# Performance work log

Measured on AMD Instinct MI355X. Metric: run time of the kernel, lower is better.

The kernel has to match this reference:

```python
import jax, jax.numpy as jnp
import numpy as np
import math

NUM_BUCKETS = 32
MAX_DISTANCE = 128
N_HEADS = 16
D_KV = 64


def _relative_position_bucket(relative_position, num_buckets=NUM_BUCKETS, max_distance=MAX_DISTANCE):
    # bidirectional (encoder) variant
    num_buckets //= 2
    relative_buckets = (relative_position > 0).astype(jnp.int32) * num_buckets
    rp = jnp.abs(relative_position)
    max_exact = num_buckets // 2
    is_small = rp < max_exact
    rp_large = max_exact + (
        jnp.log(jnp.maximum(rp, 1).astype(jnp.float32) / max_exact)
        / math.log(max_distance / max_exact)
        * (num_buckets - max_exact)
    ).astype(jnp.int32)
    rp_large = jnp.minimum(rp_large, num_buckets - 1)
    return relative_buckets + jnp.where(is_small, rp, rp_large)


def compute_bias(rel_bias, q_len, k_len):
    ctx = jnp.arange(q_len)[:, None]
    mem = jnp.arange(k_len)[None, :]
    buckets = _relative_position_bucket(mem - ctx)          # [q, k]
    values = rel_bias[buckets]                               # [q, k, h]
    return jnp.transpose(values, (2, 0, 1))[None]            # [1, h, q, k]


def setup_inputs() -> dict:
    key = jax.random.key(0)
    ks = jax.random.split(key, 6)
    d_model, inner = 1024, N_HEADS * D_KV
    s = 0.02
    return {
        "hidden_states": jax.random.normal(ks[0], (2, 2048, d_model), jnp.float32),
        "Wq": jax.random.normal(ks[1], (d_model, inner), jnp.float32) * s,
        "Wk": jax.random.normal(ks[2], (d_model, inner), jnp.float32) * s,
        "Wv": jax.random.normal(ks[3], (d_model, inner), jnp.float32) * s,
        "Wo": jax.random.normal(ks[4], (inner, d_model), jnp.float32) * s,
        "rel_bias": jax.random.normal(ks[5], (NUM_BUCKETS, N_HEADS), jnp.float32) * s,
    }


def reference(hidden_states, Wq, Wk, Wv, Wo, rel_bias):
    B, S, D = hidden_states.shape

    def split_heads(x):  # [B,S,inner] -> [B,H,S,dk]
        return x.reshape(B, S, N_HEADS, D_KV).transpose(0, 2, 1, 3)

    q = split_heads(hidden_states @ Wq)
    k = split_heads(hidden_states @ Wk)
    v = split_heads(hidden_states @ Wv)

    # T5 does NOT scale by 1/sqrt(d_kv)
    scores = jnp.einsum("bhqd,bhkd->bhqk", q, k)
    scores = scores + compute_bias(rel_bias, S, S)
    attn = jax.nn.softmax(scores, axis=-1)
    ctx = jnp.einsum("bhqk,bhkd->bhqd", attn, v)
    ctx = ctx.transpose(0, 2, 1, 3).reshape(B, S, N_HEADS * D_KV)
    return ctx @ Wo
```

## Files before the change

kernel.cpp:

```cpp
#include <hip/hip_runtime.h>
#include <hip/hip_bf16.h>

typedef __bf16 bf16x8 __attribute__((ext_vector_type(8)));
typedef __bf16 bf16x4 __attribute__((ext_vector_type(4)));
typedef float floatx4 __attribute__((ext_vector_type(4)));
using bf16 = __hip_bfloat16;

#define S_    2048
#define NHEAD 16
#define LOG2E 1.4426950408889634f

__device__ __forceinline__ void load_lds16(const bf16* g, void* lds) {
  __builtin_amdgcn_global_load_lds((const __attribute__((address_space(1))) void*)g,
                                   (__attribute__((address_space(3))) void*)lds, 16, 0, 0);
}

__global__ void prep_kernel(const float* __restrict__ hidden,
                            const float* __restrict__ wq, const float* __restrict__ wk,
                            const float* __restrict__ wv, const float* __restrict__ wo,
                            const float* __restrict__ rel_bias,
                            bf16* __restrict__ hbf, bf16* __restrict__ wt_qkv,
                            bf16* __restrict__ wt_o, float* __restrict__ btab) {
  __shared__ bf16 tile[32][33];
  int bx = blockIdx.x, t = threadIdx.x;
  if (bx < 2048) {
    int i = (bx * 256 + t) * 8;
    float4 v0 = *(const float4*)(hidden + i);
    float4 v1 = *(const float4*)(hidden + i + 4);
    bf16 o8[8] = {__float2bfloat16(v0.x), __float2bfloat16(v0.y),
                  __float2bfloat16(v0.z), __float2bfloat16(v0.w),
                  __float2bfloat16(v1.x), __float2bfloat16(v1.y),
                  __float2bfloat16(v1.z), __float2bfloat16(v1.w)};
    *(uint4*)(hbf + i) = *(const uint4*)o8;
  } else if (bx < 6144) {
    int mat = (bx - 2048) >> 10, tb = (bx - 2048) & 1023;
    int n0 = (tb & 31) * 32, k0 = (tb >> 5) * 32;
    const float* src = (mat == 0) ? wq : (mat == 1) ? wk : (mat == 2) ? wv : wo;
    bf16* dst = (mat == 3) ? wt_o : wt_qkv + mat * 1024 * 1024;
    int tx = t & 31, ty = t >> 5;
#pragma unroll
    for (int j = 0; j < 32; j += 8)
      tile[ty + j][tx] = __float2bfloat16(src[(k0 + ty + j) * 1024 + n0 + tx]);
    __syncthreads();
#pragma unroll
    for (int j = 0; j < 32; j += 8)
      dst[(n0 + ty + j) * 1024 + k0 + tx] = tile[tx][ty + j];
  } else {
    int idx = (bx - 6144) * 256 + t;
    int h = idx >> 12, j = idx & 4095;
    int delta = j - 2048;
    int rb = (delta > 0) ? 16 : 0;
    int rpa = delta < 0 ? -delta : delta;
    int bsmall;
    if (rpa < 8) {
      bsmall = rpa;
    } else {
      int lg = 25 - __clz(rpa * rpa);
      bsmall = 8 + lg;
      if (bsmall > 15) bsmall = 15;
    }
    btab[idx] = rel_bias[(rb + bsmall) * 16 + h] * LOG2E;
  }
}

__global__ __launch_bounds__(256) void gemm_qkv_kernel(const bf16* __restrict__ A,
                                                       const bf16* __restrict__ Bt,
                                                       bf16* __restrict__ qh,
                                                       bf16* __restrict__ kf,
                                                       bf16* __restrict__ vf) {
  const int K = 1024;
  __shared__ bf16 As[128 * 32];
  __shared__ bf16 Bs[128 * 32];
  int t = threadIdx.x;
  int m0 = blockIdx.y * 128, n0 = blockIdx.x * 128;
  int w = t >> 6, lane = t & 63, ln = lane & 15, quad = lane >> 4;
  int wr = w >> 1, wc = w & 1;
  floatx4 acc[4][4];
  floatx4 zero = {0.f, 0.f, 0.f, 0.f};
#pragma unroll
  for (int i = 0; i < 4; i++)
#pragma unroll
    for (int j = 0; j < 4; j++) acc[i][j] = zero;

  int r = t >> 2, c = (t & 3) * 8;
  const bf16* Ag = A + (long)(m0 + r) * K + c;
  const bf16* Bg = Bt + (long)(n0 + r) * K + c;
  char* ldsA0 = (char*)As + w * 1024;
  char* ldsA1 = ldsA0 + 4096;
  char* ldsB0 = (char*)Bs + w * 1024;
  char* ldsB1 = ldsB0 + 4096;

  for (int k0 = 0; k0 < K; k0 += 32) {
    load_lds16(Ag + k0, ldsA0);
    load_lds16(Ag + (long)64 * K + k0, ldsA1);
    load_lds16(Bg + k0, ldsB0);
    load_lds16(Bg + (long)64 * K + k0, ldsB1);
    __syncthreads();
    bf16x8 af[4], bfv[4];
#pragma unroll
    for (int i = 0; i < 4; i++)
      af[i] = *(const bf16x8*)&As[(wr * 64 + i * 16 + ln) * 32 + quad * 8];
#pragma unroll
    for (int j = 0; j < 4; j++)
      bfv[j] = *(const bf16x8*)&Bs[(wc * 64 + j * 16 + ln) * 32 + quad * 8];
#pragma unroll
    for (int i = 0; i < 4; i++)
#pragma unroll
      for (int j = 0; j < 4; j++)
        acc[i][j] = __builtin_amdgcn_mfma_f32_16x16x32_bf16(af[i], bfv[j], acc[i][j], 0, 0, 0);
    __syncthreads();
  }

  int nb = n0 + wc * 64;
  int type = nb >> 10, h = (nb >> 6) & 15;
  int b = (m0 >> 11);
  int sl0 = (m0 & 2047) + wr * 64;
  long bhbase = (long)((b * 16 + h)) * 131072;

  if (type == 0) {
#pragma unroll
    for (int i = 0; i < 4; i++)
#pragma unroll
      for (int j = 0; j < 4; j++) {
        int d = j * 16 + ln;
#pragma unroll
        for (int rr = 0; rr < 4; rr++) {
          int s = sl0 + i * 16 + quad * 4 + rr;
          qh[bhbase + (long)s * 64 + d] = __float2bfloat16(acc[i][j][rr]);
        }
      }
  } else if (type == 1) {
#pragma unroll
    for (int i = 0; i < 4; i++)
#pragma unroll
      for (int j = 0; j < 4; j++) {
        int d = j * 16 + ln;
        int dpart = (d >> 5) * 512 + ((d >> 3) & 3) * 128 + (d & 7);
        int kb = (sl0 + i * 16) * 64;
#pragma unroll
        for (int rr = 0; rr < 4; rr++)
          kf[bhbase + kb + dpart + (quad * 4 + rr) * 8] = __float2bfloat16(acc[i][j][rr]);
      }
  } else {
#pragma unroll
    for (int i = 0; i < 4; i++)
#pragma unroll
      for (int j = 0; j < 4; j++) {
        int off = (sl0 + (i >> 1) * 32) * 64 + j * 512 +
                  ((quad >> 1) + ((i & 1) << 1)) * 128 + ln * 8 + (quad & 1) * 4;
        bf16x4 pk = {(__bf16)acc[i][j][0], (__bf16)acc[i][j][1],
                     (__bf16)acc[i][j][2], (__bf16)acc[i][j][3]};
        *(bf16x4*)(vf + bhbase + off) = pk;
      }
  }
}

__global__ __launch_bounds__(256, 2) void attn_kernel(const bf16* __restrict__ qh,
                                                      const bf16* __restrict__ kf,
                                                      const bf16* __restrict__ vf,
                                                      const float* __restrict__ btab,
                                                      float* __restrict__ opart,
                                                      float* __restrict__ lpart) {
  __shared__ char KV[2][16384];
  __shared__ char PsRaw[4 * 2048];
  int t = threadIdx.x, w = t >> 6, lane = t & 63, ln = lane & 15, quad = lane >> 4;
  int bh = blockIdx.x, h = bh & 15;
  int qw = blockIdx.y * 128 + w * 32;
  int ks = blockIdx.z, kbase0 = ks * 1024;

  const bf16* qbase = qh + (long)bh * S_ * 64;
  const bf16* kfb = kf + (long)bh * S_ * 64 + (long)kbase0 * 64;
  const bf16* vfb = vf + (long)bh * S_ * 64 + (long)kbase0 * 64;
  const float* bt = btab + h * 4096;
  char* myPs = PsRaw + w * 2048;
  int lbo = quad * 256 + ln * 16;

  bf16x8 Qf[2][2];
#pragma unroll
  for (int g = 0; g < 2; g++) {
    const bf16* qr = qbase + (long)(qw + g * 16 + ln) * 64;
    Qf[g][0] = *(const bf16x8*)(qr + quad * 8);
    Qf[g][1] = *(const bf16x8*)(qr + 32 + quad * 8);
  }

  float cneg = bt[0], cpos = bt[4095];
  float l_acc[2] = {0.f, 0.f};
  floatx4 o[2][4];
  floatx4 zero = {0.f, 0.f, 0.f, 0.f};
#pragma unroll
  for (int g = 0; g < 2; g++)
#pragma unroll
    for (int dt = 0; dt < 4; dt++) o[g][dt] = zero;

  load_lds16(kfb + t * 8, KV[0] + w * 1024);
  load_lds16(kfb + 2048 + t * 8, KV[0] + 4096 + w * 1024);
  load_lds16(vfb + t * 8, KV[0] + 8192 + w * 1024);
  load_lds16(vfb + 2048 + t * 8, KV[0] + 12288 + w * 1024);

  int pb = 0;
  for (int it = 0; it < 16; it++) {
    int k0 = kbase0 + it * 64;
    __syncthreads();
    if (it < 15) {
      const bf16* kg = kfb + (it + 1) * 4096 + t * 8;
      const bf16* vg = vfb + (it + 1) * 4096 + t * 8;
      char* nb_ = KV[pb ^ 1];
      load_lds16(kg, nb_ + w * 1024);
      load_lds16(kg + 2048, nb_ + 4096 + w * 1024);
      load_lds16(vg, nb_ + 8192 + w * 1024);
      load_lds16(vg + 2048, nb_ + 12288 + w * 1024);
    }

    const char* bK = KV[pb];
    const char* bV = KV[pb] + 8192;
    bf16x8 Kr[4][2], Vr[4][2];
#pragma unroll
    for (int tile = 0; tile < 4; tile++) {
      Kr[tile][0] = *(const bf16x8*)(bK + tile * 2048 + lbo);
      Kr[tile][1] = *(const bf16x8*)(bK + tile * 2048 + 1024 + lbo);
    }
#pragma unroll
    for (int f = 0; f < 2; f++)
#pragma unroll
      for (int dt = 0; dt < 4; dt++)
        Vr[dt][f] = *(const bf16x8*)(bV + f * 4096 + dt * 1024 + lbo);

    bool near = (k0 > qw - 192) && (k0 < qw + 160);
#pragma unroll
    for (int g = 0; g < 2; g++) {
      floatx4 st[4];
#pragma unroll
      for (int tile = 0; tile < 4; tile++) {
        st[tile] = __builtin_amdgcn_mfma_f32_16x16x32_bf16(Kr[tile][0], Qf[g][0], zero, 0, 0, 0);
        st[tile] = __builtin_amdgcn_mfma_f32_16x16x32_bf16(Kr[tile][1], Qf[g][1], st[tile], 0, 0, 0);
      }
      if (near) {
#pragma unroll
        for (int tile = 0; tile < 4; tile++) {
          int bidx = k0 + tile * 16 + quad * 4 - (qw + g * 16 + ln) + 2048;
          float p0 = __builtin_amdgcn_exp2f(fmaf(st[tile][0], LOG2E, bt[bidx + 0]));
          float p1 = __builtin_amdgcn_exp2f(fmaf(st[tile][1], LOG2E, bt[bidx + 1]));
          float p2 = __builtin_amdgcn_exp2f(fmaf(st[tile][2], LOG2E, bt[bidx + 2]));
          float p3 = __builtin_amdgcn_exp2f(fmaf(st[tile][3], LOG2E, bt[bidx + 3]));
          l_acc[g] += (p0 + p1) + (p2 + p3);
          bf16x4 pk = {(__bf16)p0, (__bf16)p1, (__bf16)p2, (__bf16)p3};
          int chunk = tile * 2 + (quad >> 1);
          *(bf16x4*)(myPs + (ln * 8 + (chunk ^ (ln & 7))) * 16 + (quad & 1) * 8) = pk;
        }
      } else {
        float cb = (k0 > qw) ? cpos : cneg;
#pragma unroll
        for (int tile = 0; tile < 4; tile++) {
          float p0 = __builtin_amdgcn_exp2f(fmaf(st[tile][0], LOG2E, cb));
          float p1 = __builtin_amdgcn_exp2f(fmaf(st[tile][1], LOG2E, cb));
          float p2 = __builtin_amdgcn_exp2f(fmaf(st[tile][2], LOG2E, cb));
          float p3 = __builtin_amdgcn_exp2f(fmaf(st[tile][3], LOG2E, cb));
          l_acc[g] += (p0 + p1) + (p2 + p3);
          bf16x4 pk = {(__bf16)p0, (__bf16)p1, (__bf16)p2, (__bf16)p3};
          int chunk = tile * 2 + (quad >> 1);
          *(bf16x4*)(myPs + (ln * 8 + (chunk ^ (ln & 7))) * 16 + (quad & 1) * 8) = pk;
        }
      }

      bf16x8 Pf0 = *(const bf16x8*)(myPs + (ln * 8 + (quad ^ (ln & 7))) * 16);
      bf16x8 Pf1 = *(const bf16x8*)(myPs + (ln * 8 + ((4 + quad) ^ (ln & 7))) * 16);
#pragma unroll
      for (int dt = 0; dt < 4; dt++) {
        o[g][dt] = __builtin_amdgcn_mfma_f32_16x16x32_bf16(Pf0, Vr[dt][0], o[g][dt], 0, 0, 0);
        o[g][dt] = __builtin_amdgcn_mfma_f32_16x16x32_bf16(Pf1, Vr[dt][1], o[g][dt], 0, 0, 0);
      }
    }
    pb ^= 1;
  }

  long obase = ((long)(ks * 32 + bh)) * S_ * 64;
#pragma unroll
  for (int g = 0; g < 2; g++) {
    l_acc[g] += __shfl_xor(l_acc[g], 16);
    l_acc[g] += __shfl_xor(l_acc[g], 32);
    if (quad == 0)
      lpart[(long)(ks * 32 + bh) * S_ + qw + g * 16 + ln] = l_acc[g];
#pragma unroll
    for (int rr = 0; rr < 4; rr++) {
      int q = qw + g * 16 + quad * 4 + rr;
#pragma unroll
      for (int dt = 0; dt < 4; dt++)
        opart[obase + (long)q * 64 + dt * 16 + ln] = o[g][dt][rr];
    }
  }
}

__global__ void reduce_kernel(const float* __restrict__ opart,
                              const float* __restrict__ lpart,
                              bf16* __restrict__ ctx) {
  long flat = ((long)blockIdx.x * 256 + threadIdx.x) * 4;
  int d = flat & 63;
  int q = (int)((flat >> 6) & 2047);
  int bh = (int)(flat >> 17);
  long base = ((long)bh * S_ + q) * 64 + d;
  float4 o0 = *(const float4*)(opart + base);
  float4 o1 = *(const float4*)(opart + 4194304 + base);
  float inv = 1.0f / (lpart[(long)bh * S_ + q] + lpart[65536 + (long)bh * S_ + q]);
  bf16x4 pk = {(__bf16)((o0.x + o1.x) * inv), (__bf16)((o0.y + o1.y) * inv),
               (__bf16)((o0.z + o1.z) * inv), (__bf16)((o0.w + o1.w) * inv)};
  *(bf16x4*)(ctx + ((long)((bh >> 4) * S_ + q)) * 1024 + (bh & 15) * 64 + d) = pk;
}

__global__ __launch_bounds__(256) void gemm_bt_kernel(const bf16* __restrict__ A,
                                                      const bf16* __restrict__ Bt,
                                                      float* __restrict__ C,
                                                      int M, int N, int K) {
  __shared__ bf16 As[128 * 32];
  __shared__ bf16 Bs[128 * 32];
  int t = threadIdx.x;
  int m0 = blockIdx.y * 128, n0 = blockIdx.x * 128;
  int w = t >> 6, lane = t & 63, ln = lane & 15, quad = lane >> 4;
  int wr = w >> 1, wc = w & 1;
  floatx4 acc[4][4];
  floatx4 zero = {0.f, 0.f, 0.f, 0.f};
#pragma unroll
  for (int i = 0; i < 4; i++)
#pragma unroll
    for (int j = 0; j < 4; j++) acc[i][j] = zero;

  int r = t >> 2, c = (t & 3) * 8;
  const bf16* Ag = A + (long)(m0 + r) * K + c;
  const bf16* Bg = Bt + (long)(n0 + r) * K + c;
  char* ldsA0 = (char*)As + w * 1024;
  char* ldsA1 = ldsA0 + 4096;
  char* ldsB0 = (char*)Bs + w * 1024;
  char* ldsB1 = ldsB0 + 4096;

  for (int k0 = 0; k0 < K; k0 += 32) {
    load_lds16(Ag + k0, ldsA0);
    load_lds16(Ag + (long)64 * K + k0, ldsA1);
    load_lds16(Bg + k0, ldsB0);
    load_lds16(Bg + (long)64 * K + k0, ldsB1);
    __syncthreads();
    bf16x8 af[4], bfv[4];
#pragma unroll
    for (int i = 0; i < 4; i++)
      af[i] = *(const bf16x8*)&As[(wr * 64 + i * 16 + ln) * 32 + quad * 8];
#pragma unroll
    for (int j = 0; j < 4; j++)
      bfv[j] = *(const bf16x8*)&Bs[(wc * 64 + j * 16 + ln) * 32 + quad * 8];
#pragma unroll
    for (int i = 0; i < 4; i++)
#pragma unroll
      for (int j = 0; j < 4; j++)
        acc[i][j] = __builtin_amdgcn_mfma_f32_16x16x32_bf16(af[i], bfv[j], acc[i][j], 0, 0, 0);
    __syncthreads();
  }

#pragma unroll
  for (int i = 0; i < 4; i++)
#pragma unroll
    for (int j = 0; j < 4; j++)
#pragma unroll
      for (int rr = 0; rr < 4; rr++)
        C[(long)(m0 + wr * 64 + i * 16 + quad * 4 + rr) * N + n0 + wc * 64 + j * 16 + ln] =
            acc[i][j][rr];
}

extern "C" void kernel_launch(void* const* d_in, const int* in_sizes, int n_in,
                              void* d_out, int out_size, void* d_ws, size_t ws_size,
                              hipStream_t stream) {
  (void)in_sizes; (void)n_in; (void)out_size; (void)ws_size;
  const float* hidden   = (const float*)d_in[0];
  const float* Wq       = (const float*)d_in[1];
  const float* Wk       = (const float*)d_in[2];
  const float* Wv       = (const float*)d_in[3];
  const float* Wo       = (const float*)d_in[4];
  const float* rel_bias = (const float*)d_in[5];

  char* ws = (char*)d_ws;
  bf16*  hbf    = (bf16*)(ws + 0);
  bf16*  wt_qkv = (bf16*)(ws + 8388608);
  bf16*  wt_o   = (bf16*)(ws + 14680064);
  float* btab   = (float*)(ws + 16777216);
  bf16*  qh     = (bf16*)(ws + 17039360);
  bf16*  kf     = (bf16*)(ws + 25427968);
  bf16*  vf     = (bf16*)(ws + 33816576);
  bf16*  ctx    = (bf16*)(ws + 42205184);
  float* opart  = (float*)(ws + 50593792);
  float* lpart  = (float*)(ws + 84148224);

  prep_kernel<<<dim3(6400), dim3(256), 0, stream>>>(hidden, Wq, Wk, Wv, Wo, rel_bias,
                                                    hbf, wt_qkv, wt_o, btab);
  gemm_qkv_kernel<<<dim3(24, 32), dim3(256), 0, stream>>>(hbf, wt_qkv, qh, kf, vf);
  attn_kernel<<<dim3(32, 16, 2), dim3(256), 0, stream>>>(qh, kf, vf, btab, opart, lpart);
  reduce_kernel<<<dim3(4096), dim3(256), 0, stream>>>(opart, lpart, ctx);
  gemm_bt_kernel<<<dim3(8, 32), dim3(256), 0, stream>>>(ctx, wt_o, (float*)d_out, 4096, 1024, 1024);
}
```

Measured before the change: 206.4 us.

## Shrink GEMM tiles to 128x64 and load K/V directly into registers

Both GEMMs now use a 128x64 output tile, with each wave computing a 32x64 strip, and launch twice as many blocks. The aim is better occupancy and more blocks across the CUs, at the cost of less operand reuse per block. The attention kernel no longer stages K/V through LDS with global_load_lds and barriers. Each wave loads its K/V fragments straight from global memory into registers, prefetches the next tile, and separates the P write phase from the PV MFMA phase using a larger per-wave P buffer. This removes block-level syncs, but every wave in a block now reads K/V redundantly and register pressure rises.

After: 211.3 us. 1.02x slower.

```diff
diff --git a/kernel.cpp b/kernel.cpp
--- a/kernel.cpp
+++ b/kernel.cpp
@@ -70,15 +70,14 @@
                                                        bf16* __restrict__ vf) {
   const int K = 1024;
   __shared__ bf16 As[128 * 32];
-  __shared__ bf16 Bs[128 * 32];
+  __shared__ bf16 Bs[64 * 32];
   int t = threadIdx.x;
-  int m0 = blockIdx.y * 128, n0 = blockIdx.x * 128;
+  int m0 = blockIdx.y * 128, n0 = blockIdx.x * 64;
   int w = t >> 6, lane = t & 63, ln = lane & 15, quad = lane >> 4;
-  int wr = w >> 1, wc = w & 1;
-  floatx4 acc[4][4];
+  floatx4 acc[2][4];
   floatx4 zero = {0.f, 0.f, 0.f, 0.f};
 #pragma unroll
-  for (int i = 0; i < 4; i++)
+  for (int i = 0; i < 2; i++)
 #pragma unroll
     for (int j = 0; j < 4; j++) acc[i][j] = zero;
 
@@ -88,38 +87,35 @@
   char* ldsA0 = (char*)As + w * 1024;
   char* ldsA1 = ldsA0 + 4096;
   char* ldsB0 = (char*)Bs + w * 1024;
-  char* ldsB1 = ldsB0 + 4096;
 
   for (int k0 = 0; k0 < K; k0 += 32) {
     load_lds16(Ag + k0, ldsA0);
     load_lds16(Ag + (long)64 * K + k0, ldsA1);
     load_lds16(Bg + k0, ldsB0);
-    load_lds16(Bg + (long)64 * K + k0, ldsB1);
-    __syncthreads();
-    bf16x8 af[4], bfv[4];
-#pragma unroll
-    for (int i = 0; i < 4; i++)
-      af[i] = *(const bf16x8*)&As[(wr * 64 + i * 16 + ln) * 32 + quad * 8];
+    __syncthreads();
+    bf16x8 af[2], bfv[4];
+#pragma unroll
+    for (int i = 0; i < 2; i++)
+      af[i] = *(const bf16x8*)&As[(w * 32 + i * 16 + ln) * 32 + quad * 8];
 #pragma unroll
     for (int j = 0; j < 4; j++)
-      bfv[j] = *(const bf16x8*)&Bs[(wc * 64 + j * 16 + ln) * 32 + quad * 8];
-#pragma unroll
-    for (int i = 0; i < 4; i++)
+      bfv[j] = *(const bf16x8*)&Bs[(j * 16 + ln) * 32 + quad * 8];
+#pragma unroll
+    for (int i = 0; i < 2; i++)
 #pragma unroll
       for (int j = 0; j < 4; j++)
         acc[i][j] = __builtin_amdgcn_mfma_f32_16x16x32_bf16(af[i], bfv[j], acc[i][j], 0, 0, 0);
     __syncthreads();
   }
 
-  int nb = n0 + wc * 64;
-  int type = nb >> 10, h = (nb >> 6) & 15;
-  int b = (m0 >> 11);
-  int sl0 = (m0 & 2047) + wr * 64;
-  long bhbase = (long)((b * 16 + h)) * 131072;
+  int type = n0 >> 10, h = (n0 >> 6) & 15;
+  int b = m0 >> 11;
+  int sl0 = (m0 & 2047) + w * 32;
+  long bhbase = (long)(b * 16 + h) * 131072;
 
   if (type == 0) {
 #pragma unroll
-    for (int i = 0; i < 4; i++)
+    for (int i = 0; i < 2; i++)
 #pragma unroll
       for (int j = 0; j < 4; j++) {
         int d = j * 16 + ln;
@@ -131,7 +127,7 @@
       }
   } else if (type == 1) {
 #pragma unroll
-    for (int i = 0; i < 4; i++)
+    for (int i = 0; i < 2; i++)
 #pragma unroll
       for (int j = 0; j < 4; j++) {
         int d = j * 16 + ln;
@@ -143,11 +139,10 @@
       }
   } else {
 #pragma unroll
-    for (int i = 0; i < 4; i++)
+    for (int i = 0; i < 2; i++)
 #pragma unroll
       for (int j = 0; j < 4; j++) {
-        int off = (sl0 + (i >> 1) * 32) * 64 + j * 512 +
-                  ((quad >> 1) + ((i & 1) << 1)) * 128 + ln * 8 + (quad & 1) * 4;
+        int off = sl0 * 64 + j * 512 + ((quad >> 1) + (i << 1)) * 128 + ln * 8 + (quad & 1) * 4;
         bf16x4 pk = {(__bf16)acc[i][j][0], (__bf16)acc[i][j][1],
                      (__bf16)acc[i][j][2], (__bf16)acc[i][j][3]};
         *(bf16x4*)(vf + bhbase + off) = pk;
@@ -161,19 +156,18 @@
                                                       const float* __restrict__ btab,
                                                       float* __restrict__ opart,
                                                       float* __restrict__ lpart) {
-  __shared__ char KV[2][16384];
-  __shared__ char PsRaw[4 * 2048];
+  __shared__ char PsRaw[4 * 4096];
   int t = threadIdx.x, w = t >> 6, lane = t & 63, ln = lane & 15, quad = lane >> 4;
   int bh = blockIdx.x, h = bh & 15;
   int qw = blockIdx.y * 128 + w * 32;
-  int ks = blockIdx.z, kbase0 = ks * 1024;
+  int ks = blockIdx.z, kb0 = ks * 1024;
 
   const bf16* qbase = qh + (long)bh * S_ * 64;
-  const bf16* kfb = kf + (long)bh * S_ * 64 + (long)kbase0 * 64;
-  const bf16* vfb = vf + (long)bh * S_ * 64 + (long)kbase0 * 64;
+  const bf16* kfb = kf + (long)bh * S_ * 64 + (long)kb0 * 64;
+  const bf16* vfb = vf + (long)bh * S_ * 64 + (long)kb0 * 64;
   const float* bt = btab + h * 4096;
-  char* myPs = PsRaw + w * 2048;
-  int lbo = quad * 256 + ln * 16;
+  char* myPs = PsRaw + w * 4096;
+  int foff = quad * 128 + ln * 8;
 
   bf16x8 Qf[2][2];
 #pragma unroll
@@ -192,47 +186,45 @@
 #pragma unroll
     for (int dt = 0; dt < 4; dt++) o[g][dt] = zero;
 
-  load_lds16(kfb + t * 8, KV[0] + w * 1024);
-  load_lds16(kfb + 2048 + t * 8, KV[0] + 4096 + w * 1024);
-  load_lds16(vfb + t * 8, KV[0] + 8192 + w * 1024);
-  load_lds16(vfb + 2048 + t * 8, KV[0] + 12288 + w * 1024);
-
-  int pb = 0;
+  bf16x8 Kc[4][2], Vc[4][2];
+#pragma unroll
+  for (int tile = 0; tile < 4; tile++) {
+    Kc[tile][0] = *(const bf16x8*)(kfb + tile * 1024 + foff);
+    Kc[tile][1] = *(const bf16x8*)(kfb + tile * 1024 + 512 + foff);
+  }
+#pragma unroll
+  for (int f = 0; f < 2; f++)
+#pragma unroll
+    for (int dt = 0; dt < 4; dt++)
+      Vc[dt][f] = *(const bf16x8*)(vfb + f * 2048 + dt * 512 + foff);
+
   for (int it = 0; it < 16; it++) {
-    int k0 = kbase0 + it * 64;
-    __syncthreads();
+    int k0 = kb0 + it * 64;
+    bf16x8 Kn[4][2], Vn[4][2];
     if (it < 15) {
-      const bf16* kg = kfb + (it + 1) * 4096 + t * 8;
-      const bf16* vg = vfb + (it + 1) * 4096 + t * 8;
-      char* nb_ = KV[pb ^ 1];
-      load_lds16(kg, nb_ + w * 1024);
-      load_lds16(kg + 2048, nb_ + 4096 + w * 1024);
-      load_lds16(vg, nb_ + 8192 + w * 1024);
-      load_lds16(vg + 2048, nb_ + 12288 + w * 1024);
-    }
-
-    const char* bK = KV[pb];
-    const char* bV = KV[pb] + 8192;
-    bf16x8 Kr[4][2], Vr[4][2];
-#pragma unroll
-    for (int tile = 0; tile < 4; tile++) {
-      Kr[tile][0] = *(const bf16x8*)(bK + tile * 2048 + lbo);
-      Kr[tile][1] = *(const bf16x8*)(bK + tile * 2048 + 1024 + lbo);
-    }
-#pragma unroll
-    for (int f = 0; f < 2; f++)
-#pragma unroll
-      for (int dt = 0; dt < 4; dt++)
-        Vr[dt][f] = *(const bf16x8*)(bV + f * 4096 + dt * 1024 + lbo);
+      const bf16* kp = kfb + (it + 1) * 4096;
+      const bf16* vp = vfb + (it + 1) * 4096;
+#pragma unroll
+      for (int tile = 0; tile < 4; tile++) {
+        Kn[tile][0] = *(const bf16x8*)(kp + tile * 1024 + foff);
+        Kn[tile][1] = *(const bf16x8*)(kp + tile * 1024 + 512 + foff);
+      }
+#pragma unroll
+      for (int f = 0; f < 2; f++)
+#pragma unroll
+        for (int dt = 0; dt < 4; dt++)
+          Vn[dt][f] = *(const bf16x8*)(vp + f * 2048 + dt * 512 + foff);
+    }
 
     bool near = (k0 > qw - 192) && (k0 < qw + 160);
 #pragma unroll
     for (int g = 0; g < 2; g++) {
+      char* ps = myPs + g * 2048;
       floatx4 st[4];
 #pragma unroll
       for (int tile = 0; tile < 4; tile++) {
-        st[tile] = __builtin_amdgcn_mfma_f32_16x16x32_bf16(Kr[tile][0], Qf[g][0], zero, 0, 0, 0);
-        st[tile] = __builtin_amdgcn_mfma_f32_16x16x32_bf16(Kr[tile][1], Qf[g][1], st[tile], 0, 0, 0);
+        st[tile] = __builtin_amdgcn_mfma_f32_16x16x32_bf16(Kc[tile][0], Qf[g][0], zero, 0, 0, 0);
+        st[tile] = __builtin_amdgcn_mfma_f32_16x16x32_bf16(Kc[tile][1], Qf[g][1], st[tile], 0, 0, 0);
       }
       if (near) {
 #pragma unroll
@@ -245,7 +237,7 @@
           l_acc[g] += (p0 + p1) + (p2 + p3);
           bf16x4 pk = {(__bf16)p0, (__bf16)p1, (__bf16)p2, (__bf16)p3};
           int chunk = tile * 2 + (quad >> 1);
-          *(bf16x4*)(myPs + (ln * 8 + (chunk ^ (ln & 7))) * 16 + (quad & 1) * 8) = pk;
+          *(bf16x4*)(ps + (ln * 8 + (chunk ^ (ln & 7))) * 16 + (quad & 1) * 8) = pk;
         }
       } else {
         float cb = (k0 > qw) ? cpos : cneg;
@@ -258,19 +250,30 @@
           l_acc[g] += (p0 + p1) + (p2 + p3);
           bf16x4 pk = {(__bf16)p0, (__bf16)p1, (__bf16)p2, (__bf16)p3};
           int chunk = tile * 2 + (quad >> 1);
-          *(bf16x4*)(myPs + (ln * 8 + (chunk ^ (ln & 7))) * 16 + (quad & 1) * 8) = pk;
+          *(bf16x4*)(ps + (ln * 8 + (chunk ^ (ln & 7))) * 16 + (quad & 1) * 8) = pk;
         }
       }
-
-      bf16x8 Pf0 = *(const bf16x8*)(myPs + (ln * 8 + (quad ^ (ln & 7))) * 16);
-      bf16x8 Pf1 = *(const bf16x8*)(myPs + (ln * 8 + ((4 + quad) ^ (ln & 7))) * 16);
+    }
+
+#pragma unroll
+    for (int g = 0; g < 2; g++) {
+      char* ps = myPs + g * 2048;
+      bf16x8 Pf0 = *(const bf16x8*)(ps + (ln * 8 + (quad ^ (ln & 7))) * 16);
+      bf16x8 Pf1 = *(const bf16x8*)(ps + (ln * 8 + ((4 + quad) ^ (ln & 7))) * 16);
 #pragma unroll
       for (int dt = 0; dt < 4; dt++) {
-        o[g][dt] = __builtin_amdgcn_mfma_f32_16x16x32_bf16(Pf0, Vr[dt][0], o[g][dt], 0, 0, 0);
-        o[g][dt] = __builtin_amdgcn_mfma_f32_16x16x32_bf16(Pf1, Vr[dt][1], o[g][dt], 0, 0, 0);
-      }
-    }
-    pb ^= 1;
+        o[g][dt] = __builtin_amdgcn_mfma_f32_16x16x32_bf16(Pf0, Vc[dt][0], o[g][dt], 0, 0, 0);
+        o[g][dt] = __builtin_amdgcn_mfma_f32_16x16x32_bf16(Pf1, Vc[dt][1], o[g][dt], 0, 0, 0);
+      }
+    }
+
+    if (it < 15) {
+#pragma unroll
+      for (int tile = 0; tile < 4; tile++) {
+        Kc[tile][0] = Kn[tile][0]; Kc[tile][1] = Kn[tile][1];
+        Vc[tile][0] = Vn[tile][0]; Vc[tile][1] = Vn[tile][1];
+      }
+    }
   }
 
   long obase = ((long)(ks * 32 + bh)) * S_ * 64;
@@ -311,15 +314,14 @@
                                                       float* __restrict__ C,
                                                       int M, int N, int K) {
   __shared__ bf16 As[128 * 32];
-  __shared__ bf16 Bs[128 * 32];
+  __shared__ bf16 Bs[64 * 32];
   int t = threadIdx.x;
-  int m0 = blockIdx.y * 128, n0 = blockIdx.x * 128;
+  int m0 = blockIdx.y * 128, n0 = blockIdx.x * 64;
   int w = t >> 6, lane = t & 63, ln = lane & 15, quad = lane >> 4;
-  int wr = w >> 1, wc = w & 1;
-  floatx4 acc[4][4];
+  floatx4 acc[2][4];
   floatx4 zero = {0.f, 0.f, 0.f, 0.f};
 #pragma unroll
-  for (int i = 0; i < 4; i++)
+  for (int i = 0; i < 2; i++)
 #pragma unroll
     for (int j = 0; j < 4; j++) acc[i][j] = zero;
 
@@ -329,23 +331,21 @@
   char* ldsA0 = (char*)As + w * 1024;
   char* ldsA1 = ldsA0 + 4096;
   char* ldsB0 = (char*)Bs + w * 1024;
-  char* ldsB1 = ldsB0 + 4096;
 
   for (int k0 = 0; k0 < K; k0 += 32) {
     load_lds16(Ag + k0, ldsA0);
     load_lds16(Ag + (long)64 * K + k0, ldsA1);
     load_lds16(Bg + k0, ldsB0);
-    load_lds16(Bg + (long)64 * K + k0, ldsB1);
-    __syncthreads();
-    bf16x8 af[4], bfv[4];
-#pragma unroll
-    for (int i = 0; i < 4; i++)
-      af[i] = *(const bf16x8*)&As[(wr * 64 + i * 16 + ln) * 32 + quad * 8];
+    __syncthreads();
+    bf16x8 af[2], bfv[4];
+#pragma unroll
+    for (int i = 0; i < 2; i++)
+      af[i] = *(const bf16x8*)&As[(w * 32 + i * 16 + ln) * 32 + quad * 8];
 #pragma unroll
     for (int j = 0; j < 4; j++)
-      bfv[j] = *(const bf16x8*)&Bs[(wc * 64 + j * 16 + ln) * 32 + quad * 8];
-#pragma unroll
-    for (int i = 0; i < 4; i++)
+      bfv[j] = *(const bf16x8*)&Bs[(j * 16 + ln) * 32 + quad * 8];
+#pragma unroll
+    for (int i = 0; i < 2; i++)
 #pragma unroll
       for (int j = 0; j < 4; j++)
         acc[i][j] = __builtin_amdgcn_mfma_f32_16x16x32_bf16(af[i], bfv[j], acc[i][j], 0, 0, 0);
@@ -353,12 +353,12 @@
   }
 
 #pragma unroll
-  for (int i = 0; i < 4; i++)
+  for (int i = 0; i < 2; i++)
 #pragma unroll
     for (int j = 0; j < 4; j++)
 #pragma unroll
       for (int rr = 0; rr < 4; rr++)
-        C[(long)(m0 + wr * 64 + i * 16 + quad * 4 + rr) * N + n0 + wc * 64 + j * 16 + ln] =
+        C[(long)(m0 + w * 32 + i * 16 + quad * 4 + rr) * N + n0 + j * 16 + ln] =
             acc[i][j][rr];
 }
 
@@ -387,8 +387,8 @@
 
   prep_kernel<<<dim3(6400), dim3(256), 0, stream>>>(hidden, Wq, Wk, Wv, Wo, rel_bias,
                                                     hbf, wt_qkv, wt_o, btab);
-  gemm_qkv_kernel<<<dim3(24, 32), dim3(256), 0, stream>>>(hbf, wt_qkv, qh, kf, vf);
+  gemm_qkv_kernel<<<dim3(48, 32), dim3(256), 0, stream>>>(hbf, wt_qkv, qh, kf, vf);
   attn_kernel<<<dim3(32, 16, 2), dim3(256), 0, stream>>>(qh, kf, vf, btab, opart, lpart);
   reduce_kernel<<<dim3(4096), dim3(256), 0, stream>>>(opart, lpart, ctx);
-  gemm_bt_kernel<<<dim3(8, 32), dim3(256), 0, stream>>>(ctx, wt_o, (float*)d_out, 4096, 1024, 1024);
-}
+  gemm_bt_kernel<<<dim3(16, 32), dim3(256), 0, stream>>>(ctx, wt_o, (float*)d_out, 4096, 1024, 1024);
+}
```
